# Kernel tuning notes

Hardware: AMD Instinct MI355X
Metric: run time of the kernel (lower is better)

Reference implementation:

```python
import jax, jax.numpy as jnp
import numpy as np

IN_FEATURES = 4096
OUT_FEATURES = 4096
NNZ = 1677722  # round(0.1 * 4096 * 4096)
N_TOKENS = 8192


def setup_inputs() -> dict:
    key = jax.random.key(0)
    k1, k2, k3, k4 = jax.random.split(key, 4)
    inputs = jax.random.normal(k1, (N_TOKENS, IN_FEATURES), dtype=jnp.float32)
    bound = 1.0 / IN_FEATURES ** 0.5
    weights = jax.random.uniform(k2, (NNZ,), minval=-bound, maxval=bound, dtype=jnp.float32)
    bias = jax.random.uniform(k3, (OUT_FEATURES,), minval=-bound, maxval=bound, dtype=jnp.float32)
    # COO indices: row (output) and col (input) indices, sampled like np.random.choice
    flat = jax.random.randint(k4, (NNZ,), 0, IN_FEATURES * OUT_FEATURES)
    row_ind = flat // IN_FEATURES
    col_ind = flat % IN_FEATURES
    indices = jnp.stack((row_ind, col_ind)).astype(jnp.int64)
    return {"inputs": inputs, "weights": weights, "bias": bias, "indices": indices}


def reference(inputs, weights, bias, indices):
    # Densify COO weight (duplicates are summed, matching torch coalesce/to_dense)
    dense_w = jnp.zeros((OUT_FEATURES, IN_FEATURES), dtype=weights.dtype)
    dense_w = dense_w.at[indices[0], indices[1]].add(weights)
    # output = (W @ x^T)^T + b  ==  x @ W^T + b
    out = jnp.einsum('ni,oi->no', inputs, dense_w) + bias
    return out
```

## Files before the change

### kernel.cpp

```cpp
#include <hip/hip_runtime.h>

#define M_TOK 8192
#define NF    4096
#define KF    4096
#define BK    64
#define NHALF 128

typedef __attribute__((ext_vector_type(8))) short bf16x8;
typedef __attribute__((ext_vector_type(4))) float f32x4;
typedef __attribute__((ext_vector_type(2))) short s16x2;

__device__ __forceinline__ unsigned short f2bf(float f) {
    unsigned u = __builtin_bit_cast(unsigned, f);
    u += 0x7FFFu + ((u >> 16) & 1u);
    return (unsigned short)(u >> 16);
}

__device__ __forceinline__ float bf2f(unsigned short b) {
    unsigned u = ((unsigned)b) << 16;
    return __builtin_bit_cast(float, u);
}

__device__ __forceinline__ void load_lds16(const unsigned short* g, unsigned short* l) {
    __builtin_amdgcn_global_load_lds(
        (const __attribute__((address_space(1))) unsigned int*)g,
        (__attribute__((address_space(3))) unsigned int*)l,
        16, 0, 0);
}

__device__ __forceinline__ void block_bar() {
    asm volatile("" ::: "memory");
    __builtin_amdgcn_s_barrier();
    asm volatile("" ::: "memory");
}

#define VMCNT(n) asm volatile("s_waitcnt vmcnt(" #n ")" ::: "memory")

__global__ void prep_zero_convx(const float4* __restrict__ X, ushort4* __restrict__ Xb,
                                uint4* __restrict__ Wb, int nx4, int nwb) {
    int i = blockIdx.x * blockDim.x + threadIdx.x;
    if (i < nwb) Wb[i] = (uint4){0u, 0u, 0u, 0u};
    if (i < nx4) {
        float4 v = X[i];
        ushort4 o;
        o.x = f2bf(v.x); o.y = f2bf(v.y); o.z = f2bf(v.z); o.w = f2bf(v.w);
        Xb[i] = o;
    }
}

__global__ void scatter_bf16(const int* __restrict__ idx, const float* __restrict__ w,
                             unsigned short* __restrict__ Wb, int nnz) {
    int t = blockIdx.x * blockDim.x + threadIdx.x;
    if (t >= nnz) return;
    int r = idx[t];
    int c = idx[nnz + t];
    size_t elem = (size_t)r * KF + c;
#if __has_builtin(__builtin_amdgcn_global_atomic_fadd_v2bf16)
    unsigned short wb = f2bf(w[t]);
    s16x2 val;
    if (elem & 1) { val[0] = 0; val[1] = (short)wb; }
    else          { val[0] = (short)wb; val[1] = 0; }
    __builtin_amdgcn_global_atomic_fadd_v2bf16(
        (__attribute__((address_space(1))) s16x2*)(Wb + (elem & ~(size_t)1)), val);
#else
    unsigned* addr = (unsigned*)(Wb + (elem & ~(size_t)1));
    float wf = w[t];
    unsigned old = __hip_atomic_load(addr, __ATOMIC_RELAXED, __HIP_MEMORY_SCOPE_AGENT), assumed;
    do {
        assumed = old;
        unsigned short cur = (elem & 1) ? (unsigned short)(assumed >> 16)
                                        : (unsigned short)(assumed & 0xffffu);
        unsigned short nw = f2bf(bf2f(cur) + wf);
        unsigned newv = (elem & 1) ? ((assumed & 0x0000ffffu) | ((unsigned)nw << 16))
                                   : ((assumed & 0xffff0000u) | (unsigned)nw);
        old = atomicCAS(addr, assumed, newv);
    } while (old != assumed);
#endif
}

__global__ __launch_bounds__(512, 2) void gemm_bt_bias(
    const unsigned short* __restrict__ A,
    const unsigned short* __restrict__ B,
    const float* __restrict__ bias,
    float* __restrict__ C)
{
    __shared__ unsigned short lds_u[65536];
    char* const ldsb = (char*)lds_u;

    const int tid  = threadIdx.x;
    const int lane = tid & 63;
    const int wave = tid >> 6;
    const int wm   = wave >> 2;
    const int wn   = wave & 3;

    const int flat = blockIdx.y * 32 + blockIdx.x;
    const int xcd  = flat & 7;
    const int q    = flat >> 3;
    const int bm   = (xcd & 3) * 8 + (q & 7);
    const int bn   = (xcd >> 2) * 8 + (q >> 3);

    f32x4 acc[8][4] = {};

    const int gc   = (lane & 3) ^ ((lane >> 3) & 3);
    const int srow = wave * 16 + (lane >> 2);
    const unsigned short* gA   = A + (size_t)(bm * 256 + srow) * KF + gc * 8;
    const unsigned short* gB   = B + (size_t)(bn * 256 + srow) * KF + gc * 8;
    const unsigned short* gAHi = gA + (size_t)128 * KF;
    const unsigned short* gBHi = gB + (size_t)128 * KF;

    unsigned short* const sd = lds_u + wave * 512;

    const int fr    = lane & 15;
    const int quad  = lane >> 4;
    const int pos16 = (quad ^ ((fr >> 1) & 3)) << 4;
    const int rdA   = (wm * 128 + fr) * 64 + pos16;
    const int rdB   = 16384 + (wn * 64 + fr) * 64 + pos16;

#define STAGE_A(sb, ko) do { \
    load_lds16(gA   + (ko), sd + (((sb)        ) >> 1)); \
    load_lds16(gAHi + (ko), sd + (((sb) +  8192) >> 1)); \
} while (0)
#define STAGE_B(sb, ko) do { \
    load_lds16(gB   + (ko), sd + (((sb) + 16384) >> 1)); \
    load_lds16(gBHi + (ko), sd + (((sb) + 24576) >> 1)); \
} while (0)

#define RD_A4(dst, sb, i0) do { \
    _Pragma("unroll") \
    for (int _i = 0; _i < 4; ++_i) \
        dst[_i] = *(const bf16x8*)(ldsb + (sb) + rdA + ((i0) + _i) * 1024); \
} while (0)

#define RD_B4(dst, sb) do { \
    _Pragma("unroll") \
    for (int _j = 0; _j < 4; ++_j) \
        dst[_j] = *(const bf16x8*)(ldsb + (sb) + rdB + _j * 1024); \
} while (0)

#define MFMA16(i0, af, bfv) do { \
    _Pragma("unroll") \
    for (int _i = 0; _i < 4; ++_i) \
        _Pragma("unroll") \
        for (int _j = 0; _j < 4; ++_j) \
            acc[(i0) + _i][_j] = __builtin_amdgcn_mfma_f32_16x16x32_bf16(af[_i], bfv[_j], acc[(i0) + _i][_j], 0, 0, 0); \
} while (0)

    STAGE_A(0, 0);       STAGE_B(0, 0);
    STAGE_A(32768, 32);  STAGE_B(32768, 32);
    STAGE_A(65536, 64);  STAGE_B(65536, 64);
    VMCNT(8);
    block_bar();

    int ko3 = 96;
#pragma unroll 1
    for (int g = 0; g < NHALF - 3; ++g) {
        const int sb  = (g & 3) << 15;
        const int sbn = ((g + 3) & 3) << 15;
        bf16x8 a[4], b[4];
        RD_A4(a, sb, 0);
        RD_B4(b, sb);
        STAGE_A(sbn, ko3);
        block_bar();
        __builtin_amdgcn_s_setprio(1);
        MFMA16(0, a, b);
        __builtin_amdgcn_s_setprio(0);
        block_bar();
        RD_A4(a, sb, 4);
        STAGE_B(sbn, ko3);
        block_bar();
        __builtin_amdgcn_s_setprio(1);
        MFMA16(4, a, b);
        __builtin_amdgcn_s_setprio(0);
        VMCNT(8);
        block_bar();
        ko3 += 32;
    }

    {
        bf16x8 a[4], b[4];
        RD_A4(a, 32768, 0);
        RD_B4(b, 32768);
        block_bar();
        MFMA16(0, a, b);
        block_bar();
        RD_A4(a, 32768, 4);
        block_bar();
        MFMA16(4, a, b);
        VMCNT(4);
        block_bar();
        RD_A4(a, 65536, 0);
        RD_B4(b, 65536);
        block_bar();
        MFMA16(0, a, b);
        block_bar();
        RD_A4(a, 65536, 4);
        block_bar();
        MFMA16(4, a, b);
        VMCNT(0);
        block_bar();
        RD_A4(a, 98304, 0);
        RD_B4(b, 98304);
        MFMA16(0, a, b);
        RD_A4(a, 98304, 4);
        MFMA16(4, a, b);
    }

#undef STAGE_A
#undef STAGE_B
#undef RD_A4
#undef RD_B4
#undef MFMA16

    const int crow = bm * 256 + wm * 128;
    const int ccol = bn * 256 + wn * 64;
    const int r_l  = quad * 4;
#pragma unroll
    for (int j = 0; j < 4; ++j) {
        int col = ccol + j * 16 + fr;
        float bv = bias[col];
#pragma unroll
        for (int i = 0; i < 8; ++i) {
#pragma unroll
            for (int r = 0; r < 4; ++r)
                C[(size_t)(crow + i * 16 + r_l + r) * NF + col] = acc[i][j][r] + bv;
        }
    }
}

extern "C" void kernel_launch(void* const* d_in, const int* in_sizes, int n_in,
                              void* d_out, int out_size, void* d_ws, size_t ws_size,
                              hipStream_t stream) {
    const float* x    = (const float*)d_in[0];
    const float* w    = (const float*)d_in[1];
    const float* bias = (const float*)d_in[2];
    const int*   idx  = (const int*)d_in[3];
    float* out = (float*)d_out;
    const int nnz = in_sizes[1];

    unsigned short* Wb = (unsigned short*)d_ws;
    unsigned short* Xb = (unsigned short*)((char*)d_ws + (size_t)NF * KF * sizeof(unsigned short));

    const int nx4 = M_TOK * KF / 4;
    const int nwb = NF * KF * 2 / 16;

    prep_zero_convx<<<(nx4 + 255) / 256, 256, 0, stream>>>(
        (const float4*)x, (ushort4*)Xb, (uint4*)Wb, nx4, nwb);
    scatter_bf16<<<(nnz + 255) / 256, 256, 0, stream>>>(idx, w, Wb, nnz);
    gemm_bt_bias<<<dim3(32, 16), 512, 0, stream>>>(Xb, Wb, bias, out);
}
```

Before: 537.4 us.

## Software-pipeline LDS fragment reads with one barrier per K-step

Restructures the GEMM main loop so LDS fragment loads for the next K-step are issued while MFMAs on the current step run, using double-buffered register fragments (a_lo/a_hi, b1/b2). The four barriers per iteration drop to one, and both A and B global-to-LDS stages are issued up front each step. This hides LDS read latency behind MFMA work and cuts synchronisation overhead, at the cost of more live VGPRs under a 512-thread, 2-block launch bound, which could cause spills or lower occupancy. The wait depth also changes, so correctness relies on the 4-slot ring being safe with a single barrier.

New measurement: 527.8 us. No clear change (-1.8%).

```diff
diff --git a/kernel.cpp b/kernel.cpp
--- a/kernel.cpp
+++ b/kernel.cpp
@@ -3,7 +3,6 @@
 #define M_TOK 8192
 #define NF    4096
 #define KF    4096
-#define BK    64
 #define NHALF 128
 
 typedef __attribute__((ext_vector_type(8))) short bf16x8;
@@ -125,13 +124,19 @@
     load_lds16(gBHi + (ko), sd + (((sb) + 24576) >> 1)); \
 } while (0)
 
-#define RD_A4(dst, sb, i0) do { \
+#define RD_ALO(dst, sb) do { \
     _Pragma("unroll") \
     for (int _i = 0; _i < 4; ++_i) \
-        dst[_i] = *(const bf16x8*)(ldsb + (sb) + rdA + ((i0) + _i) * 1024); \
-} while (0)
-
-#define RD_B4(dst, sb) do { \
+        dst[_i] = *(const bf16x8*)(ldsb + (sb) + rdA + _i * 1024); \
+} while (0)
+
+#define RD_AHI(dst, sb) do { \
+    _Pragma("unroll") \
+    for (int _i = 0; _i < 4; ++_i) \
+        dst[_i] = *(const bf16x8*)(ldsb + (sb) + rdA + (4 + _i) * 1024); \
+} while (0)
+
+#define RD_B(dst, sb) do { \
     _Pragma("unroll") \
     for (int _j = 0; _j < 4; ++_j) \
         dst[_j] = *(const bf16x8*)(ldsb + (sb) + rdB + _j * 1024); \
@@ -145,71 +150,73 @@
             acc[(i0) + _i][_j] = __builtin_amdgcn_mfma_f32_16x16x32_bf16(af[_i], bfv[_j], acc[(i0) + _i][_j], 0, 0, 0); \
 } while (0)
 
+    bf16x8 a_lo[4], a_hi[4], b1[4], b2[4];
+
+#define HALF(G, BC, BN) do { \
+    const int sb_  = ((G) & 3) << 15; \
+    const int sbn_ = (((G) + 1) & 3) << 15; \
+    const int sbs_ = (((G) + 3) & 3) << 15; \
+    const int ko_  = ((G) + 3) * 32; \
+    STAGE_A(sbs_, ko_); \
+    STAGE_B(sbs_, ko_); \
+    RD_AHI(a_hi, sb_); \
+    RD_B(BN, sbn_); \
+    __builtin_amdgcn_s_setprio(1); \
+    MFMA16(0, a_lo, BC); \
+    __builtin_amdgcn_s_setprio(0); \
+    RD_ALO(a_lo, sbn_); \
+    __builtin_amdgcn_s_setprio(1); \
+    MFMA16(4, a_hi, BC); \
+    __builtin_amdgcn_s_setprio(0); \
+    VMCNT(4); \
+    block_bar(); \
+} while (0)
+
     STAGE_A(0, 0);       STAGE_B(0, 0);
     STAGE_A(32768, 32);  STAGE_B(32768, 32);
     STAGE_A(65536, 64);  STAGE_B(65536, 64);
-    VMCNT(8);
+    VMCNT(4);
     block_bar();
-
-    int ko3 = 96;
+    RD_ALO(a_lo, 0);
+    RD_B(b1, 0);
+
 #pragma unroll 1
-    for (int g = 0; g < NHALF - 3; ++g) {
-        const int sb  = (g & 3) << 15;
-        const int sbn = ((g + 3) & 3) << 15;
-        bf16x8 a[4], b[4];
-        RD_A4(a, sb, 0);
-        RD_B4(b, sb);
-        STAGE_A(sbn, ko3);
-        block_bar();
+    for (int gp = 0; gp < 62; ++gp) {
+        const int g = gp * 2;
+        HALF(g,     b1, b2);
+        HALF(g + 1, b2, b1);
+    }
+    HALF(124, b1, b2);
+
+    {
+        RD_AHI(a_hi, 32768);
+        RD_B(b1, 65536);
         __builtin_amdgcn_s_setprio(1);
-        MFMA16(0, a, b);
+        MFMA16(0, a_lo, b2);
         __builtin_amdgcn_s_setprio(0);
-        block_bar();
-        RD_A4(a, sb, 4);
-        STAGE_B(sbn, ko3);
-        block_bar();
+        RD_ALO(a_lo, 65536);
         __builtin_amdgcn_s_setprio(1);
-        MFMA16(4, a, b);
+        MFMA16(4, a_hi, b2);
         __builtin_amdgcn_s_setprio(0);
-        VMCNT(8);
-        block_bar();
-        ko3 += 32;
-    }
-
-    {
-        bf16x8 a[4], b[4];
-        RD_A4(a, 32768, 0);
-        RD_B4(b, 32768);
-        block_bar();
-        MFMA16(0, a, b);
-        block_bar();
-        RD_A4(a, 32768, 4);
-        block_bar();
-        MFMA16(4, a, b);
-        VMCNT(4);
-        block_bar();
-        RD_A4(a, 65536, 0);
-        RD_B4(b, 65536);
-        block_bar();
-        MFMA16(0, a, b);
-        block_bar();
-        RD_A4(a, 65536, 4);
-        block_bar();
-        MFMA16(4, a, b);
         VMCNT(0);
         block_bar();
-        RD_A4(a, 98304, 0);
-        RD_B4(b, 98304);
-        MFMA16(0, a, b);
-        RD_A4(a, 98304, 4);
-        MFMA16(4, a, b);
+        RD_AHI(a_hi, 65536);
+        RD_B(b2, 98304);
+        MFMA16(0, a_lo, b1);
+        RD_ALO(a_lo, 98304);
+        MFMA16(4, a_hi, b1);
+        RD_AHI(a_hi, 98304);
+        MFMA16(0, a_lo, b2);
+        MFMA16(4, a_hi, b2);
     }
 
 #undef STAGE_A
 #undef STAGE_B
-#undef RD_A4
-#undef RD_B4
+#undef RD_ALO
+#undef RD_AHI
+#undef RD_B
 #undef MFMA16
+#undef HALF
 
     const int crow = bm * 256 + wm * 128;
     const int ccol = bn * 256 + wn * 64;
```
